# Kernel optimization log

Measured on AMD Instinct MI355X. Metric: run time of the kernel, lower is better.

The kernel has to match this reference:

```python
import jax, jax.numpy as jnp
import numpy as np

IN_F, OUT_F = 1024, 1024
GRID_SIZE, SPLINE_ORDER = 5, 3
BATCH = 4096
GRID_LO, GRID_HI = -1.0, 1.0


def _make_grid():
    h = (GRID_HI - GRID_LO) / GRID_SIZE
    g = jnp.arange(-SPLINE_ORDER, GRID_SIZE + SPLINE_ORDER + 1, dtype=jnp.float32) * h + GRID_LO  # [12]
    return jnp.broadcast_to(g, (IN_F, g.shape[0]))  # [in, 12]


def setup_inputs() -> dict:
    key = jax.random.key(0)
    k1, k2, k3 = jax.random.split(key, 3)
    x = jax.random.normal(k1, (BATCH, IN_F), dtype=jnp.float32)
    base_weight = jax.random.normal(k2, (OUT_F, IN_F), dtype=jnp.float32) * (1.0 / np.sqrt(IN_F))
    spline_weight = jax.random.normal(k3, (OUT_F, IN_F, GRID_SIZE + SPLINE_ORDER), dtype=jnp.float32) * 0.1
    spline_scaler = jnp.ones((OUT_F, IN_F), dtype=jnp.float32)
    grid = _make_grid()
    return {"x": x, "base_weight": base_weight, "spline_weight": spline_weight,
            "spline_scaler": spline_scaler, "grid": grid}


def b_splines(x, grid):
    # x: [B, in], grid: [in, 12] -> bases: [B, in, grid_size+spline_order]
    xe = x[..., None]  # [B, in, 1]
    bases = ((xe >= grid[:, :-1]) & (xe < grid[:, 1:])).astype(x.dtype)  # [B, in, 11]
    for k in range(1, SPLINE_ORDER + 1):
        t0 = grid[:, :-(k + 1)]
        t1 = grid[:, k:-1]
        t2 = grid[:, k + 1:]
        t3 = grid[:, 1:-k]
        bases = ((xe - t0) / (t1 - t0 + 1e-8) * bases[..., :-1]
                 + (t2 - xe) / (t2 - t3 + 1e-8) * bases[..., 1:])
    return bases


def reference(x, base_weight, spline_weight, spline_scaler, grid):
    base_output = jax.nn.silu(x) @ base_weight.T  # [B, out]
    spline_basis = b_splines(x, grid)             # [B, in, 8]
    spline_output = jnp.einsum('bij,oij,oi->bo', spline_basis, spline_weight, spline_scaler)
    return base_output + spline_output
```

## Files before the change

kernel.cpp:

```cpp
#include <hip/hip_runtime.h>
#include <hip/hip_bf16.h>
#include <stdint.h>
#include <stddef.h>

#define IN_F     1024
#define OUT_F    1024
#define BATCH    4096
#define NSPLINE  8
#define KDIM     (IN_F * 9)
#define GRIDPTS  12

typedef __bf16 bf16;
typedef __bf16 bf16x8 __attribute__((ext_vector_type(8)));
typedef float  f32x4  __attribute__((ext_vector_type(4)));

__global__ __launch_bounds__(256) void build_A(const float* __restrict__ x,
                                               const float* __restrict__ grid,
                                               bf16* __restrict__ A)
{
    __shared__ float g[GRIDPTS];
    __shared__ float rec[33];
    if (threadIdx.x < GRIDPTS) g[threadIdx.x] = grid[threadIdx.x];
    __syncthreads();
    if (threadIdx.x < 33) {
        const int k = threadIdx.x / 11 + 1;
        const int j = threadIdx.x % 11;
        if (j + k <= 11) rec[threadIdx.x] = 1.0f / (g[j + k] - g[j] + 1e-8f);
    }
    __syncthreads();

    const int idx = blockIdx.x * 256 + threadIdx.x;
    const int b = idx >> 10;
    const int i = idx & 1023;
    const float xv = x[idx];

    float bs[11];
#pragma unroll
    for (int j = 0; j < 11; ++j)
        bs[j] = (xv >= g[j] && xv < g[j + 1]) ? 1.0f : 0.0f;

#pragma unroll
    for (int k = 1; k <= 3; ++k) {
        const float* rk = &rec[(k - 1) * 11];
#pragma unroll
        for (int j = 0; j < 10; ++j) {
            if (j <= 10 - k) {
                bs[j] = (xv - g[j]) * rk[j] * bs[j]
                      + (g[j + k + 1] - xv) * rk[j + 1] * bs[j + 1];
            }
        }
    }

    const float si = xv / (1.0f + __expf(-xv));

    bf16* rowp = A + (size_t)b * KDIM;
    rowp[i] = (bf16)si;
#pragma unroll
    for (int j = 0; j < NSPLINE; ++j)
        rowp[(size_t)(j + 1) * IN_F + i] = (bf16)bs[j];
}

__global__ __launch_bounds__(256) void pack_W(const float* __restrict__ bw,
                                              const float* __restrict__ sw,
                                              const float* __restrict__ sc,
                                              bf16* __restrict__ W)
{
    const int idx = blockIdx.x * 256 + threadIdx.x;
    const int i = idx & 1023;
    const float s = sc[idx];

    bf16* rowp = W + (size_t)(idx >> 10) * KDIM;
    rowp[i] = (bf16)bw[idx];

    const float4* swv = (const float4*)(sw + (size_t)idx * NSPLINE);
    const float4 w0 = swv[0];
    const float4 w1 = swv[1];
    rowp[(size_t)1 * IN_F + i] = (bf16)(w0.x * s);
    rowp[(size_t)2 * IN_F + i] = (bf16)(w0.y * s);
    rowp[(size_t)3 * IN_F + i] = (bf16)(w0.z * s);
    rowp[(size_t)4 * IN_F + i] = (bf16)(w0.w * s);
    rowp[(size_t)5 * IN_F + i] = (bf16)(w1.x * s);
    rowp[(size_t)6 * IN_F + i] = (bf16)(w1.y * s);
    rowp[(size_t)7 * IN_F + i] = (bf16)(w1.z * s);
    rowp[(size_t)8 * IN_F + i] = (bf16)(w1.w * s);
}

#define BM8 256
#define BN8 256
#define BK8 64

#define GLOAD_LDS16(gp, lp)                                                          \
    __builtin_amdgcn_global_load_lds((const __attribute__((address_space(1))) void*)(gp), \
                                     (__attribute__((address_space(3))) void*)(lp), 16, 0, 0)

__global__ __launch_bounds__(512, 2) void gemm8(const bf16* __restrict__ A,
                                                const bf16* __restrict__ B,
                                                float* __restrict__ C,
                                                int kLen)
{
    __shared__ bf16 lds[8 * 8192];

    const int tid  = threadIdx.x;
    const int wave = tid >> 6;
    const int lane = tid & 63;

    const int nwg  = gridDim.x;
    const int q    = nwg >> 3;
    const int wgid = (blockIdx.x & 7) * q + (blockIdx.x >> 3);
    const int nxy  = (BATCH / BM8) * (OUT_F / BN8);
    const int z    = wgid / nxy;
    const int rem  = wgid - z * nxy;
    const int by   = rem >> 4;
    const int bx   = rem & 15;

    const int bm = bx * BM8;
    const int bcol = by * BN8;
    const int kBase = z * kLen;
    C += (size_t)z * BATCH * OUT_F;

    const int wr = (wave >> 2) * 128;
    const int wc = (wave & 3) * 64;

    f32x4 acc[8][4] = {};

    const int NT   = kLen / BK8;
    const int hmax = 4 * NT;

    const int srow = tid >> 2;
    const int sch  = (((tid & 3) ^ ((tid >> 3) & 3))) * 8;
    const bf16* baseA = A + (size_t)(bm + srow) * KDIM + kBase + sch;
    const bf16* baseB = B + (size_t)(bcol + srow) * KDIM + kBase + sch;
    const size_t rstep = (size_t)128 * KDIM;
    bf16* ldsw = &lds[wave * 512];

    auto stage = [&](int h) {
        if (h < hmax) {
            const int t   = h >> 2;
            const int th  = h & 3;
            const int kof = t * BK8 + ((th >> 1) ? 32 : 0);
            const bf16* src = (th & 1) ? baseB : baseA;
            bf16* l0 = ldsw + (h & 7) * 8192;
            GLOAD_LDS16(src + kof, l0);
            GLOAD_LDS16(src + kof + rstep, l0 + 4096);
        }
    };

    for (int h = 0; h < 6; ++h) stage(h);
    asm volatile("s_waitcnt vmcnt(4)" ::: "memory");
    __builtin_amdgcn_s_barrier();

    const int rowk = lane & 15;
    const int kc   = lane >> 4;
    const int kxor = (kc ^ ((rowk >> 1) & 3)) * 8;

#define LDSFRAG(slot, row) (*(const bf16x8*)&lds[(slot) * 8192 + (row) * 32 + kxor])

    bf16x8 a[4], b[4], a2[4], b2[4];
#pragma unroll
    for (int m = 0; m < 4; ++m) a[m] = LDSFRAG(0, wr + m * 16 + rowk);
#pragma unroll
    for (int n = 0; n < 4; ++n) b[n] = LDSFRAG(1, wc + n * 16 + rowk);

    for (int t = 0; t < NT; ++t) {
        const int h0  = 4 * t;
        const int sA0 = (h0 + 0) & 7;
        const int sA1 = (h0 + 2) & 7, sB1 = (h0 + 3) & 7;

        stage(h0 + 6);
#pragma unroll
        for (int m = 0; m < 4; ++m) a2[m] = LDSFRAG(sA0, wr + 64 + m * 16 + rowk);
        __builtin_amdgcn_sched_barrier(0);
        __builtin_amdgcn_s_setprio(1);
#pragma unroll
        for (int m = 0; m < 4; ++m)
#pragma unroll
            for (int n = 0; n < 4; ++n)
                acc[m][n] = __builtin_amdgcn_mfma_f32_16x16x32_bf16(a[m], b[n], acc[m][n], 0, 0, 0);
        __builtin_amdgcn_s_setprio(0);
        __builtin_amdgcn_s_barrier();

        stage(h0 + 7);
#pragma unroll
        for (int m = 0; m < 4; ++m) a[m] = LDSFRAG(sA1, wr + m * 16 + rowk);
#pragma unroll
        for (int n = 0; n < 4; ++n) b2[n] = LDSFRAG(sB1, wc + n * 16 + rowk);
        __builtin_amdgcn_sched_barrier(0);
        __builtin_amdgcn_s_setprio(1);
#pragma unroll
        for (int m = 0; m < 4; ++m)
#pragma unroll
            for (int n = 0; n < 4; ++n)
                acc[4 + m][n] = __builtin_amdgcn_mfma_f32_16x16x32_bf16(a2[m], b[n], acc[4 + m][n], 0, 0, 0);
        __builtin_amdgcn_s_setprio(0);
        __builtin_amdgcn_s_barrier();

        stage(h0 + 8);
#pragma unroll
        for (int m = 0; m < 4; ++m) a2[m] = LDSFRAG(sA1, wr + 64 + m * 16 + rowk);
        __builtin_amdgcn_sched_barrier(0);
        __builtin_amdgcn_s_setprio(1);
#pragma unroll
        for (int m = 0; m < 4; ++m)
#pragma unroll
            for (int n = 0; n < 4; ++n)
                acc[m][n] = __builtin_amdgcn_mfma_f32_16x16x32_bf16(a[m], b2[n], acc[m][n], 0, 0, 0);
        __builtin_amdgcn_s_setprio(0);
        __builtin_amdgcn_s_barrier();

        stage(h0 + 9);
        __builtin_amdgcn_sched_barrier(0);
        __builtin_amdgcn_s_setprio(1);
#pragma unroll
        for (int m = 0; m < 4; ++m)
#pragma unroll
            for (int n = 0; n < 4; ++n)
                acc[4 + m][n] = __builtin_amdgcn_mfma_f32_16x16x32_bf16(a2[m], b2[n], acc[4 + m][n], 0, 0, 0);
        __builtin_amdgcn_s_setprio(0);
        if (t < NT - 2)       asm volatile("s_waitcnt vmcnt(4)" ::: "memory");
        else if (t == NT - 2) asm volatile("s_waitcnt vmcnt(0)" ::: "memory");
        if (t + 1 < NT) {
            const int nA0 = (h0 + 4) & 7, nB0 = (h0 + 5) & 7;
#pragma unroll
            for (int m = 0; m < 4; ++m) a[m] = LDSFRAG(nA0, wr + m * 16 + rowk);
#pragma unroll
            for (int n = 0; n < 4; ++n) b[n] = LDSFRAG(nB0, wc + n * 16 + rowk);
        }
        __builtin_amdgcn_s_barrier();
    }
#undef LDSFRAG

    const int ccol = lane & 15;
    const int crow = (lane >> 4) * 4;
#pragma unroll
    for (int mf = 0; mf < 8; ++mf) {
#pragma unroll
        for (int nf = 0; nf < 4; ++nf) {
            float* cp = C + (size_t)(bm + wr + mf * 16 + crow) * OUT_F + (bcol + wc + nf * 16 + ccol);
#pragma unroll
            for (int r = 0; r < 4; ++r)
                cp[(size_t)r * OUT_F] = acc[mf][nf][r];
        }
    }
}

__global__ __launch_bounds__(256) void reduce_partials(const float4* __restrict__ P,
                                                       float4* __restrict__ out,
                                                       int nPart, int n4)
{
    const int stride = gridDim.x * 256;
    for (int i = blockIdx.x * 256 + threadIdx.x; i < n4; i += stride) {
        float4 s = P[i];
        for (int p = 1; p < nPart; ++p) {
            const float4 q = P[(size_t)p * n4 + i];
            s.x += q.x; s.y += q.y; s.z += q.z; s.w += q.w;
        }
        out[i] = s;
    }
}

extern "C" void kernel_launch(void* const* d_in, const int* in_sizes, int n_in,
                              void* d_out, int out_size, void* d_ws, size_t ws_size,
                              hipStream_t stream)
{
    const float* x  = (const float*)d_in[0];
    const float* bw = (const float*)d_in[1];
    const float* sw = (const float*)d_in[2];
    const float* sc = (const float*)d_in[3];
    const float* gr = (const float*)d_in[4];
    float* out = (float*)d_out;

    bf16* A = (bf16*)d_ws;
    bf16* W = A + (size_t)BATCH * KDIM;
    float* parts = (float*)(W + (size_t)OUT_F * KDIM);

    const size_t baseBytes = ((size_t)BATCH + OUT_F) * KDIM * sizeof(bf16);
    const size_t cBytes    = (size_t)BATCH * OUT_F * sizeof(float);

    int split = 1;
    if (ws_size >= baseBytes + 4 * cBytes)      split = 4;
    else if (ws_size >= baseBytes + 2 * cBytes) split = 2;

    build_A<<<(BATCH * IN_F) / 256, 256, 0, stream>>>(x, gr, A);
    pack_W<<<(OUT_F * IN_F) / 256, 256, 0, stream>>>(bw, sw, sc, W);

    const int nblk = (BATCH / BM8) * (OUT_F / BN8) * split;
    float* gemmOut = (split > 1) ? parts : out;
    gemm8<<<nblk, 512, 0, stream>>>(A, W, gemmOut, KDIM / split);

    if (split > 1) {
        const int n4 = BATCH * OUT_F / 4;
        reduce_partials<<<2048, 256, 0, stream>>>((const float4*)parts, (float4*)out,
                                                  split, n4);
    }
}
```

Baseline: 122.2 us.

## Switch GEMM inner loop to 32x32x16 bf16 MFMA with reordered pipeline

Replaces the 16x16x32 MFMA tiles with 32x32x16 bf16 MFMA, so each wave's 128x64 tile is covered by 4x2 larger accumulators. LDS fragment loads, the swizzle offsets and the output store mapping are rewritten to match the new operand and accumulator layouts. Barriers are moved ahead of the fragment loads and the stage issue order is reshuffled. The aim is fewer MFMA issues and fewer LDS reads per K step. The cost is a different register footprint and a new barrier/wait ordering that has to stay correct.

```diff
diff --git a/kernel.cpp b/kernel.cpp
--- a/kernel.cpp
+++ b/kernel.cpp
@@ -12,7 +12,7 @@
 
 typedef __bf16 bf16;
 typedef __bf16 bf16x8 __attribute__((ext_vector_type(8)));
-typedef float  f32x4  __attribute__((ext_vector_type(4)));
+typedef float  f32x16 __attribute__((ext_vector_type(16)));
 
 __global__ __launch_bounds__(256) void build_A(const float* __restrict__ x,
                                                const float* __restrict__ grid,
@@ -113,7 +113,7 @@
     const int by   = rem >> 4;
     const int bx   = rem & 15;
 
-    const int bm = bx * BM8;
+    const int bm   = bx * BM8;
     const int bcol = by * BN8;
     const int kBase = z * kLen;
     C += (size_t)z * BATCH * OUT_F;
@@ -121,7 +121,7 @@
     const int wr = (wave >> 2) * 128;
     const int wc = (wave & 3) * 64;
 
-    f32x4 acc[8][4] = {};
+    f32x16 acc[4][2] = {};
 
     const int NT   = kLen / BK8;
     const int hmax = 4 * NT;
@@ -149,96 +149,103 @@
     asm volatile("s_waitcnt vmcnt(4)" ::: "memory");
     __builtin_amdgcn_s_barrier();
 
-    const int rowk = lane & 15;
-    const int kc   = lane >> 4;
-    const int kxor = (kc ^ ((rowk >> 1) & 3)) * 8;
-
-#define LDSFRAG(slot, row) (*(const bf16x8*)&lds[(slot) * 8192 + (row) * 32 + kxor])
-
-    bf16x8 a[4], b[4], a2[4], b2[4];
-#pragma unroll
-    for (int m = 0; m < 4; ++m) a[m] = LDSFRAG(0, wr + m * 16 + rowk);
-#pragma unroll
-    for (int n = 0; n < 4; ++n) b[n] = LDSFRAG(1, wc + n * 16 + rowk);
+    const int l31  = lane & 31;
+    const int rsw  = (lane >> 1) & 3;
+    const int offE = (((lane >> 5) + 0) ^ rsw) * 8;
+    const int offO = (((lane >> 5) + 2) ^ rsw) * 8;
+
+#define LDSFRAG(slot, row, off) (*(const bf16x8*)&lds[(slot) * 8192 + (row) * 32 + (off)])
+
+    bf16x8 a[4], b[2], a2[4], b2[2];
+#pragma unroll
+    for (int m = 0; m < 4; ++m) a[m] = LDSFRAG(0, wr + m * 32 + l31, offE);
+#pragma unroll
+    for (int n = 0; n < 2; ++n) b[n] = LDSFRAG(1, wc + n * 32 + l31, offE);
 
     for (int t = 0; t < NT; ++t) {
         const int h0  = 4 * t;
-        const int sA0 = (h0 + 0) & 7;
+        const int sA0 = (h0 + 0) & 7, sB0 = (h0 + 1) & 7;
         const int sA1 = (h0 + 2) & 7, sB1 = (h0 + 3) & 7;
 
         stage(h0 + 6);
-#pragma unroll
-        for (int m = 0; m < 4; ++m) a2[m] = LDSFRAG(sA0, wr + 64 + m * 16 + rowk);
+        __builtin_amdgcn_s_barrier();
+#pragma unroll
+        for (int m = 0; m < 4; ++m) a2[m] = LDSFRAG(sA0, wr + m * 32 + l31, offO);
+#pragma unroll
+        for (int n = 0; n < 2; ++n) b2[n] = LDSFRAG(sB0, wc + n * 32 + l31, offO);
         __builtin_amdgcn_sched_barrier(0);
         __builtin_amdgcn_s_setprio(1);
 #pragma unroll
         for (int m = 0; m < 4; ++m)
 #pragma unroll
-            for (int n = 0; n < 4; ++n)
-                acc[m][n] = __builtin_amdgcn_mfma_f32_16x16x32_bf16(a[m], b[n], acc[m][n], 0, 0, 0);
+            for (int n = 0; n < 2; ++n)
+                acc[m][n] = __builtin_amdgcn_mfma_f32_32x32x16_bf16(a[m], b[n], acc[m][n], 0, 0, 0);
         __builtin_amdgcn_s_setprio(0);
+
+        stage(h0 + 7);
         __builtin_amdgcn_s_barrier();
-
-        stage(h0 + 7);
-#pragma unroll
-        for (int m = 0; m < 4; ++m) a[m] = LDSFRAG(sA1, wr + m * 16 + rowk);
-#pragma unroll
-        for (int n = 0; n < 4; ++n) b2[n] = LDSFRAG(sB1, wc + n * 16 + rowk);
+#pragma unroll
+        for (int m = 0; m < 4; ++m) a[m] = LDSFRAG(sA1, wr + m * 32 + l31, offE);
+#pragma unroll
+        for (int n = 0; n < 2; ++n) b[n] = LDSFRAG(sB1, wc + n * 32 + l31, offE);
         __builtin_amdgcn_sched_barrier(0);
         __builtin_amdgcn_s_setprio(1);
 #pragma unroll
         for (int m = 0; m < 4; ++m)
 #pragma unroll
-            for (int n = 0; n < 4; ++n)
-                acc[4 + m][n] = __builtin_amdgcn_mfma_f32_16x16x32_bf16(a2[m], b[n], acc[4 + m][n], 0, 0, 0);
+            for (int n = 0; n < 2; ++n)
+                acc[m][n] = __builtin_amdgcn_mfma_f32_32x32x16_bf16(a2[m], b2[n], acc[m][n], 0, 0, 0);
         __builtin_amdgcn_s_setprio(0);
+
+        stage(h0 + 8);
         __builtin_amdgcn_s_barrier();
-
-        stage(h0 + 8);
-#pragma unroll
-        for (int m = 0; m < 4; ++m) a2[m] = LDSFRAG(sA1, wr + 64 + m * 16 + rowk);
+#pragma unroll
+        for (int m = 0; m < 4; ++m) a2[m] = LDSFRAG(sA1, wr + m * 32 + l31, offO);
+#pragma unroll
+        for (int n = 0; n < 2; ++n) b2[n] = LDSFRAG(sB1, wc + n * 32 + l31, offO);
         __builtin_amdgcn_sched_barrier(0);
         __builtin_amdgcn_s_setprio(1);
 #pragma unroll
         for (int m = 0; m < 4; ++m)
 #pragma unroll
-            for (int n = 0; n < 4; ++n)
-                acc[m][n] = __builtin_amdgcn_mfma_f32_16x16x32_bf16(a[m], b2[n], acc[m][n], 0, 0, 0);
+            for (int n = 0; n < 2; ++n)
+                acc[m][n] = __builtin_amdgcn_mfma_f32_32x32x16_bf16(a[m], b[n], acc[m][n], 0, 0, 0);
         __builtin_amdgcn_s_setprio(0);
+
+        stage(h0 + 9);
+        if (t < NT - 2)       asm volatile("s_waitcnt vmcnt(4)" ::: "memory");
+        else if (t == NT - 2) asm volatile("s_waitcnt vmcnt(0)" ::: "memory");
         __builtin_amdgcn_s_barrier();
-
-        stage(h0 + 9);
+        if (t + 1 < NT) {
+            const int nA0 = (h0 + 4) & 7, nB0 = (h0 + 5) & 7;
+#pragma unroll
+            for (int m = 0; m < 4; ++m) a[m] = LDSFRAG(nA0, wr + m * 32 + l31, offE);
+#pragma unroll
+            for (int n = 0; n < 2; ++n) b[n] = LDSFRAG(nB0, wc + n * 32 + l31, offE);
+        }
         __builtin_amdgcn_sched_barrier(0);
         __builtin_amdgcn_s_setprio(1);
 #pragma unroll
         for (int m = 0; m < 4; ++m)
 #pragma unroll
-            for (int n = 0; n < 4; ++n)
-                acc[4 + m][n] = __builtin_amdgcn_mfma_f32_16x16x32_bf16(a2[m], b2[n], acc[4 + m][n], 0, 0, 0);
+            for (int n = 0; n < 2; ++n)
+                acc[m][n] = __builtin_amdgcn_mfma_f32_32x32x16_bf16(a2[m], b2[n], acc[m][n], 0, 0, 0);
         __builtin_amdgcn_s_setprio(0);
-        if (t < NT - 2)       asm volatile("s_waitcnt vmcnt(4)" ::: "memory");
-        else if (t == NT - 2) asm volatile("s_waitcnt vmcnt(0)" ::: "memory");
-        if (t + 1 < NT) {
-            const int nA0 = (h0 + 4) & 7, nB0 = (h0 + 5) & 7;
-#pragma unroll
-            for (int m = 0; m < 4; ++m) a[m] = LDSFRAG(nA0, wr + m * 16 + rowk);
-#pragma unroll
-            for (int n = 0; n < 4; ++n) b[n] = LDSFRAG(nB0, wc + n * 16 + rowk);
-        }
-        __builtin_amdgcn_s_barrier();
     }
 #undef LDSFRAG
 
-    const int ccol = lane & 15;
-    const int crow = (lane >> 4) * 4;
-#pragma unroll
-    for (int mf = 0; mf < 8; ++mf) {
-#pragma unroll
-        for (int nf = 0; nf < 4; ++nf) {
-            float* cp = C + (size_t)(bm + wr + mf * 16 + crow) * OUT_F + (bcol + wc + nf * 16 + ccol);
-#pragma unroll
-            for (int r = 0; r < 4; ++r)
-                cp[(size_t)r * OUT_F] = acc[mf][nf][r];
+    const int ccol = l31;
+    const int rhi  = 4 * (lane >> 5);
+#pragma unroll
+    for (int mf = 0; mf < 4; ++mf) {
+#pragma unroll
+        for (int nf = 0; nf < 2; ++nf) {
+            float* cp = C + (size_t)(bm + wr + mf * 32 + rhi) * OUT_F + (bcol + wc + nf * 32 + ccol);
+#pragma unroll
+            for (int reg = 0; reg < 16; ++reg) {
+                const int rl = (reg & 3) + 8 * (reg >> 2);
+                cp[(size_t)rl * OUT_F] = acc[mf][nf][reg];
+            }
         }
     }
 }
```

New measurement: 127.8 us. 4.6% more time.

## Fuse prep kernels and replace split-K partial reduction with atomic adds

Applied to the files above, without the earlier changes.

Merges build_A and pack_W into one launch that branches on block index. Replaces the split-K partial-sum buffers and the separate reduce kernel with a memset of the output followed by atomic float adds from each K-split. This removes a kernel launch and the write/read of four partial 16 MB buffers, but adds contended atomic traffic and makes the summation order non-deterministic.

```diff
diff --git a/kernel.cpp b/kernel.cpp
--- a/kernel.cpp
+++ b/kernel.cpp
@@ -14,80 +14,85 @@
 typedef __bf16 bf16x8 __attribute__((ext_vector_type(8)));
 typedef float  f32x4  __attribute__((ext_vector_type(4)));
 
-__global__ __launch_bounds__(256) void build_A(const float* __restrict__ x,
-                                               const float* __restrict__ grid,
-                                               bf16* __restrict__ A)
+#define NB_BUILD (BATCH * IN_F / 256)
+#define NB_PACK  (OUT_F * IN_F / 256)
+
+__global__ __launch_bounds__(256) void prep(const float* __restrict__ x,
+                                            const float* __restrict__ grid,
+                                            const float* __restrict__ bw,
+                                            const float* __restrict__ sw,
+                                            const float* __restrict__ sc,
+                                            bf16* __restrict__ A,
+                                            bf16* __restrict__ W)
 {
     __shared__ float g[GRIDPTS];
     __shared__ float rec[33];
-    if (threadIdx.x < GRIDPTS) g[threadIdx.x] = grid[threadIdx.x];
-    __syncthreads();
-    if (threadIdx.x < 33) {
-        const int k = threadIdx.x / 11 + 1;
-        const int j = threadIdx.x % 11;
-        if (j + k <= 11) rec[threadIdx.x] = 1.0f / (g[j + k] - g[j] + 1e-8f);
+
+    if (blockIdx.x < NB_BUILD) {
+        if (threadIdx.x < GRIDPTS) g[threadIdx.x] = grid[threadIdx.x];
+        __syncthreads();
+        if (threadIdx.x < 33) {
+            const int k = threadIdx.x / 11 + 1;
+            const int j = threadIdx.x % 11;
+            if (j + k <= 11) rec[threadIdx.x] = 1.0f / (g[j + k] - g[j] + 1e-8f);
+        }
+        __syncthreads();
+
+        const int idx = blockIdx.x * 256 + threadIdx.x;
+        const int b = idx >> 10;
+        const int i = idx & 1023;
+        const float xv = x[idx];
+
+        float bs[11];
+#pragma unroll
+        for (int j = 0; j < 11; ++j)
+            bs[j] = (xv >= g[j] && xv < g[j + 1]) ? 1.0f : 0.0f;
+
+#pragma unroll
+        for (int k = 1; k <= 3; ++k) {
+            const float* rk = &rec[(k - 1) * 11];
+#pragma unroll
+            for (int j = 0; j < 10; ++j) {
+                if (j <= 10 - k) {
+                    bs[j] = (xv - g[j]) * rk[j] * bs[j]
+                          + (g[j + k + 1] - xv) * rk[j + 1] * bs[j + 1];
+                }
+            }
+        }
+
+        const float si = xv / (1.0f + __expf(-xv));
+
+        bf16* rowp = A + (size_t)b * KDIM;
+        rowp[i] = (bf16)si;
+#pragma unroll
+        for (int j = 0; j < NSPLINE; ++j)
+            rowp[(size_t)(j + 1) * IN_F + i] = (bf16)bs[j];
+    } else {
+        const int idx = (blockIdx.x - NB_BUILD) * 256 + threadIdx.x;
+        const int i = idx & 1023;
+        const float s = sc[idx];
+
+        bf16* rowp = W + (size_t)(idx >> 10) * KDIM;
+        rowp[i] = (bf16)bw[idx];
+
+        const float4* swv = (const float4*)(sw + (size_t)idx * NSPLINE);
+        const float4 w0 = swv[0];
+        const float4 w1 = swv[1];
+        rowp[(size_t)1 * IN_F + i] = (bf16)(w0.x * s);
+        rowp[(size_t)2 * IN_F + i] = (bf16)(w0.y * s);
+        rowp[(size_t)3 * IN_F + i] = (bf16)(w0.z * s);
+        rowp[(size_t)4 * IN_F + i] = (bf16)(w0.w * s);
+        rowp[(size_t)5 * IN_F + i] = (bf16)(w1.x * s);
+        rowp[(size_t)6 * IN_F + i] = (bf16)(w1.y * s);
+        rowp[(size_t)7 * IN_F + i] = (bf16)(w1.z * s);
+        rowp[(size_t)8 * IN_F + i] = (bf16)(w1.w * s);
     }
-    __syncthreads();
-
-    const int idx = blockIdx.x * 256 + threadIdx.x;
-    const int b = idx >> 10;
-    const int i = idx & 1023;
-    const float xv = x[idx];
-
-    float bs[11];
-#pragma unroll
-    for (int j = 0; j < 11; ++j)
-        bs[j] = (xv >= g[j] && xv < g[j + 1]) ? 1.0f : 0.0f;
-
-#pragma unroll
-    for (int k = 1; k <= 3; ++k) {
-        const float* rk = &rec[(k - 1) * 11];
-#pragma unroll
-        for (int j = 0; j < 10; ++j) {
-            if (j <= 10 - k) {
-                bs[j] = (xv - g[j]) * rk[j] * bs[j]
-                      + (g[j + k + 1] - xv) * rk[j + 1] * bs[j + 1];
-            }
-        }
-    }
-
-    const float si = xv / (1.0f + __expf(-xv));
-
-    bf16* rowp = A + (size_t)b * KDIM;
-    rowp[i] = (bf16)si;
-#pragma unroll
-    for (int j = 0; j < NSPLINE; ++j)
-        rowp[(size_t)(j + 1) * IN_F + i] = (bf16)bs[j];
-}
-
-__global__ __launch_bounds__(256) void pack_W(const float* __restrict__ bw,
-                                              const float* __restrict__ sw,
-                                              const float* __restrict__ sc,
-                                              bf16* __restrict__ W)
-{
-    const int idx = blockIdx.x * 256 + threadIdx.x;
-    const int i = idx & 1023;
-    const float s = sc[idx];
-
-    bf16* rowp = W + (size_t)(idx >> 10) * KDIM;
-    rowp[i] = (bf16)bw[idx];
-
-    const float4* swv = (const float4*)(sw + (size_t)idx * NSPLINE);
-    const float4 w0 = swv[0];
-    const float4 w1 = swv[1];
-    rowp[(size_t)1 * IN_F + i] = (bf16)(w0.x * s);
-    rowp[(size_t)2 * IN_F + i] = (bf16)(w0.y * s);
-    rowp[(size_t)3 * IN_F + i] = (bf16)(w0.z * s);
-    rowp[(size_t)4 * IN_F + i] = (bf16)(w0.w * s);
-    rowp[(size_t)5 * IN_F + i] = (bf16)(w1.x * s);
-    rowp[(size_t)6 * IN_F + i] = (bf16)(w1.y * s);
-    rowp[(size_t)7 * IN_F + i] = (bf16)(w1.z * s);
-    rowp[(size_t)8 * IN_F + i] = (bf16)(w1.w * s);
 }
 
 #define BM8 256
 #define BN8 256
 #define BK8 64
+#define SPLIT 4
 
 #define GLOAD_LDS16(gp, lp)                                                          \
     __builtin_amdgcn_global_load_lds((const __attribute__((address_space(1))) void*)(gp), \
@@ -113,10 +118,9 @@
     const int by   = rem >> 4;
     const int bx   = rem & 15;
 
-    const int bm = bx * BM8;
+    const int bm   = bx * BM8;
     const int bcol = by * BN8;
     const int kBase = z * kLen;
-    C += (size_t)z * BATCH * OUT_F;
 
     const int wr = (wave >> 2) * 128;
     const int wc = (wave & 3) * 64;
@@ -238,23 +242,8 @@
             float* cp = C + (size_t)(bm + wr + mf * 16 + crow) * OUT_F + (bcol + wc + nf * 16 + ccol);
 #pragma unroll
             for (int r = 0; r < 4; ++r)
-                cp[(size_t)r * OUT_F] = acc[mf][nf][r];
-        }
-    }
-}
-
-__global__ __launch_bounds__(256) void reduce_partials(const float4* __restrict__ P,
-                                                       float4* __restrict__ out,
-                                                       int nPart, int n4)
-{
-    const int stride = gridDim.x * 256;
-    for (int i = blockIdx.x * 256 + threadIdx.x; i < n4; i += stride) {
-        float4 s = P[i];
-        for (int p = 1; p < nPart; ++p) {
-            const float4 q = P[(size_t)p * n4 + i];
-            s.x += q.x; s.y += q.y; s.z += q.z; s.w += q.w;
-        }
-        out[i] = s;
+                unsafeAtomicAdd(cp + (size_t)r * OUT_F, acc[mf][nf][r]);
+        }
     }
 }
 
@@ -271,25 +260,11 @@
 
     bf16* A = (bf16*)d_ws;
     bf16* W = A + (size_t)BATCH * KDIM;
-    float* parts = (float*)(W + (size_t)OUT_F * KDIM);
-
-    const size_t baseBytes = ((size_t)BATCH + OUT_F) * KDIM * sizeof(bf16);
-    const size_t cBytes    = (size_t)BATCH * OUT_F * sizeof(float);
-
-    int split = 1;
-    if (ws_size >= baseBytes + 4 * cBytes)      split = 4;
-    else if (ws_size >= baseBytes + 2 * cBytes) split = 2;
-
-    build_A<<<(BATCH * IN_F) / 256, 256, 0, stream>>>(x, gr, A);
-    pack_W<<<(OUT_F * IN_F) / 256, 256, 0, stream>>>(bw, sw, sc, W);
-
-    const int nblk = (BATCH / BM8) * (OUT_F / BN8) * split;
-    float* gemmOut = (split > 1) ? parts : out;
-    gemm8<<<nblk, 512, 0, stream>>>(A, W, gemmOut, KDIM / split);
-
-    if (split > 1) {
-        const int n4 = BATCH * OUT_F / 4;
-        reduce_partials<<<2048, 256, 0, stream>>>((const float4*)parts, (float4*)out,
-                                                  split, n4);
-    }
+
+    hipMemsetAsync(d_out, 0, (size_t)BATCH * OUT_F * sizeof(float), stream);
+
+    prep<<<NB_BUILD + NB_PACK, 256, 0, stream>>>(x, gr, bw, sw, sc, A, W);
+
+    const int nblk = (BATCH / BM8) * (OUT_F / BN8) * SPLIT;
+    gemm8<<<nblk, 512, 0, stream>>>(A, W, out, KDIM / SPLIT);
 }
```

Result: slower. 154.0 us (+26.1%).
